# Optimization experiments

Measured on AMD Instinct MI355X. Metric: run time of the kernel, lower is better.

Reference implementation:

```python
import jax, jax.numpy as jnp
import numpy as np

B, S, T, D, H, K, F = 8, 512, 512, 1024, 16, 64, 4096
EPS = 1e-6
NEG = -1e9


def _ln(x, g, b):
    mu = jnp.mean(x, axis=-1, keepdims=True)
    var = jnp.mean(jnp.square(x - mu), axis=-1, keepdims=True)
    return (x - mu) * jax.lax.rsqrt(var + EPS) * g + b


def _mha(q_in, kv_in, wq, bq, wk, bk, wv, bv, wo, bo, mask=None):
    # q_in: [B,S,D], kv_in: [B,T,D]
    q = jnp.einsum('bsd,dhk->bshk', q_in, wq) + bq
    k = jnp.einsum('btd,dhk->bthk', kv_in, wk) + bk
    v = jnp.einsum('btd,dhk->bthk', kv_in, wv) + bv
    scores = jnp.einsum('bshk,bthk->bhst', q, k) / jnp.sqrt(jnp.float32(K))
    if mask is not None:
        scores = jnp.where(mask, scores, NEG)
    attn = jax.nn.softmax(scores, axis=-1)  # [B,H,S,T]
    ctx = jnp.einsum('bhst,bthk->bshk', attn, v)
    out = jnp.einsum('bshk,hkd->bsd', ctx, wo) + bo
    return out, attn


def setup_inputs() -> dict:
    key = jax.random.key(0)
    ks = jax.random.split(key, 24)
    r = lambda i, shape: 0.02 * jax.random.normal(ks[i], shape, dtype=jnp.float32)
    inp = {
        'x': jax.random.normal(ks[0], (B, S, D), dtype=jnp.float32),
        'enc_output': jax.random.normal(ks[1], (B, T, D), dtype=jnp.float32),
        'look_ahead_mask': jnp.tril(jnp.ones((S, S), dtype=bool))[None, None],
        # mha1 (self-attention)
        'wq1': r(2, (D, H, K)), 'bq1': jnp.zeros((H, K), jnp.float32),
        'wk1': r(3, (D, H, K)), 'bk1': jnp.zeros((H, K), jnp.float32),
        'wv1': r(4, (D, H, K)), 'bv1': jnp.zeros((H, K), jnp.float32),
        'wo1': r(5, (H, K, D)), 'bo1': jnp.zeros((D,), jnp.float32),
        # mha2 (cross-attention)
        'wq2': r(6, (D, H, K)), 'bq2': jnp.zeros((H, K), jnp.float32),
        'wk2': r(7, (D, H, K)), 'bk2': jnp.zeros((H, K), jnp.float32),
        'wv2': r(8, (D, H, K)), 'bv2': jnp.zeros((H, K), jnp.float32),
        'wo2': r(9, (H, K, D)), 'bo2': jnp.zeros((D,), jnp.float32),
        # layernorms
        'g1': jnp.ones((D,), jnp.float32), 'be1': jnp.zeros((D,), jnp.float32),
        'g2': jnp.ones((D,), jnp.float32), 'be2': jnp.zeros((D,), jnp.float32),
        'g3': jnp.ones((D,), jnp.float32), 'be3': jnp.zeros((D,), jnp.float32),
        # ffn
        'w_fc1': r(10, (D, F)), 'b_fc1': jnp.zeros((F,), jnp.float32),
        'w_fc2': r(11, (F, D)), 'b_fc2': jnp.zeros((D,), jnp.float32),
    }
    return inp


def reference(x, enc_output, look_ahead_mask,
              wq1, bq1, wk1, bk1, wv1, bv1, wo1, bo1,
              wq2, bq2, wk2, bk2, wv2, bv2, wo2, bo2,
              g1, be1, g2, be2, g3, be3,
              w_fc1, b_fc1, w_fc2, b_fc2):
    attn1, attn_w1 = _mha(x, x, wq1, bq1, wk1, bk1, wv1, bv1, wo1, bo1,
                          mask=look_ahead_mask)
    out1 = _ln(attn1 + x, g1, be1)
    attn2, attn_w2 = _mha(out1, enc_output, wq2, bq2, wk2, bk2, wv2, bv2, wo2, bo2)
    out2 = _ln(attn2 + out1, g2, be2)
    h = jax.nn.relu(jnp.einsum('bsd,df->bsf', out2, w_fc1) + b_fc1)
    out_ffn = jnp.einsum('bsf,fd->bsd', h, w_fc2) + b_fc2
    dec_layer_out = _ln(out_ffn + out2, g3, be3)
    return dec_layer_out, attn_w1, attn_w2
```

## Files before the change

kernel.cpp:

```cpp
#include <hip/hip_runtime.h>

typedef __attribute__((ext_vector_type(4))) float f32x4;
typedef __attribute__((ext_vector_type(8))) __bf16 bf16x8;

__device__ __forceinline__ unsigned short f2b(float f){
  union { float f; unsigned int u; } v; v.f = f;
  unsigned int r = v.u + 0x7FFFu + ((v.u >> 16) & 1u);
  return (unsigned short)(r >> 16);
}
__device__ __forceinline__ float b2f(unsigned short u){
  union { unsigned int u; float f; } v; v.u = ((unsigned int)u) << 16;
  return v.f;
}
__device__ __forceinline__ bool in_is_bf16(const void* g1){
  return ((const unsigned short*)g1)[0] == 0x3F80u;
}

#define GLD16(gp, lp) __builtin_amdgcn_global_load_lds( \
    (const __attribute__((address_space(1))) unsigned int*)(gp), \
    (__attribute__((address_space(3))) unsigned int*)(lp), 16, 0, 0)

__global__ __launch_bounds__(256) void k_fill(float* p, long long n, float v){
  long long i = (long long)blockIdx.x*256 + threadIdx.x;
  long long stride = (long long)gridDim.x*256;
  for(; i < n; i += stride) p[i] = v;
}

struct SmallConv { const void* src[16]; int n[16]; int off[16]; };
struct TW4 { const void* s[4]; };

template<bool SMALL>
__global__ __launch_bounds__(256) void k_prepA(SmallConv sc, float* bias,
    const void* act_in, unsigned short* act_out,
    TW4 tw, unsigned short* wdst, const void* g1f)
{
  __shared__ float tile[32][33];
  bool isb = in_is_bf16(g1f);
  int bi = blockIdx.x, tid = threadIdx.x;
  int base = SMALL ? 16 : 0;
  if(SMALL && bi < 16){
    const void* s = sc.src[bi];
    float* d = bias + sc.off[bi];
    int n = sc.n[bi];
    for(int j=tid;j<n;j+=256)
      d[j] = isb ? b2f(((const unsigned short*)s)[j]) : ((const float*)s)[j];
  } else if(bi < base + 2048){
    for(int i=(bi-base)*256+tid; i<4194304; i+=2048*256){
      float v = isb ? b2f(((const unsigned short*)act_in)[i]) : ((const float*)act_in)[i];
      act_out[i] = f2b(v);
    }
  } else {
    int r = bi - (base + 2048);
    int wi = r >> 10, rem = r & 1023;
    int c0 = (rem & 31)*32, r0 = (rem >> 5)*32;
    const void* src = tw.s[wi];
    unsigned short* dst = wdst + (size_t)wi*1048576;
    int tx = tid & 31, ty = tid >> 5;
    for(int rr=ty; rr<32; rr+=8){
      size_t o = (size_t)(r0+rr)*1024 + c0 + tx;
      tile[rr][tx] = isb ? b2f(((const unsigned short*)src)[o]) : ((const float*)src)[o];
    }
    __syncthreads();
    for(int cc=ty; cc<32; cc+=8)
      dst[(size_t)(c0+cc)*1024 + r0 + tx] = f2b(tile[tx][cc]);
  }
}

__global__ __launch_bounds__(256) void k_prep3(
    const void* fc1, unsigned short* fc1t,
    const void* fc2, unsigned short* fc2t, const void* g1f)
{
  __shared__ float tile[32][33];
  bool isb = in_is_bf16(g1f);
  int bi = blockIdx.x, tid = threadIdx.x;
  const void* src; unsigned short* dst; int R, C, bx, by;
  if(bi < 4096){ src = fc1; dst = fc1t; R = 1024; C = 4096; bx = bi & 127; by = bi >> 7; }
  else { int r = bi - 4096; src = fc2; dst = fc2t; R = 4096; C = 1024; bx = r & 31; by = r >> 5; }
  int c0 = bx*32, r0 = by*32;
  int tx = tid & 31, ty = tid >> 5;
  for(int rr=ty; rr<32; rr+=8){
    size_t o = (size_t)(r0+rr)*C + c0 + tx;
    tile[rr][tx] = isb ? b2f(((const unsigned short*)src)[o]) : ((const float*)src)[o];
  }
  __syncthreads();
  for(int cc=ty; cc<32; cc+=8)
    dst[(size_t)(c0+cc)*R + r0 + tx] = f2b(tile[tx][cc]);
}

template<int EPI>
__global__ __launch_bounds__(256) void k_gemm(
    const unsigned short* __restrict__ A, int lda,
    const unsigned short* __restrict__ Bt, int ldb,
    void* __restrict__ Cout, int ldc,
    const float* __restrict__ bias, const unsigned short* __restrict__ resid, int K)
{
  __shared__ unsigned short As[2][128*32];
  __shared__ unsigned short Bs[2][128*32];
  int tid = threadIdx.x;
  int lane = tid & 63, w = tid >> 6;
  int lr = lane & 15, lg = lane >> 4;
  int m0 = blockIdx.y * 128, n0 = blockIdx.x * 128;
  int wr = w >> 1, wc = w & 1;

  f32x4 acc[4][4];
  #pragma unroll
  for(int m=0;m<4;m++)
    #pragma unroll
    for(int n=0;n<4;n++) acc[m][n] = (f32x4){0.f,0.f,0.f,0.f};

  #pragma unroll
  for(int j=0;j<2;j++){
    int idx = j*256 + tid;
    GLD16(A + (size_t)(m0 + (idx>>2))*lda + (idx&3)*8,
          As[0] + (size_t)(j*256 + (tid & 192))*8);
    GLD16(Bt + (size_t)(n0 + (idx>>2))*ldb + (idx&3)*8,
          Bs[0] + (size_t)(j*256 + (tid & 192))*8);
  }
  __syncthreads();

  int cur = 0;
  for(int k0 = 0; k0 < K; k0 += 32){
    if(k0 + 32 < K){
      #pragma unroll
      for(int j=0;j<2;j++){
        int idx = j*256 + tid;
        GLD16(A + (size_t)(m0 + (idx>>2))*lda + k0 + 32 + (idx&3)*8,
              As[cur^1] + (size_t)(j*256 + (tid & 192))*8);
        GLD16(Bt + (size_t)(n0 + (idx>>2))*ldb + k0 + 32 + (idx&3)*8,
              Bs[cur^1] + (size_t)(j*256 + (tid & 192))*8);
      }
    }
    bf16x8 a[4], b[4];
    #pragma unroll
    for(int m=0;m<4;m++) a[m] = *(const bf16x8*)&As[cur][(wr*64 + m*16 + lr)*32 + lg*8];
    #pragma unroll
    for(int n=0;n<4;n++) b[n] = *(const bf16x8*)&Bs[cur][(wc*64 + n*16 + lr)*32 + lg*8];
    #pragma unroll
    for(int m=0;m<4;m++)
      #pragma unroll
      for(int n=0;n<4;n++)
        acc[m][n] = __builtin_amdgcn_mfma_f32_16x16x32_bf16(a[m], b[n], acc[m][n], 0,0,0);
    __syncthreads();
    cur ^= 1;
  }

  #pragma unroll
  for(int m=0;m<4;m++){
    #pragma unroll
    for(int n=0;n<4;n++){
      int col = n0 + wc*64 + n*16 + lr;
      float bb = bias[col];
      #pragma unroll
      for(int r=0;r<4;r++){
        int row = m0 + wr*64 + m*16 + lg*4 + r;
        size_t o = (size_t)row*ldc + col;
        float v = acc[m][n][r] + bb;
        if constexpr (EPI == 0){
          ((unsigned short*)Cout)[o] = f2b(v);
        } else if constexpr (EPI == 1){
          ((unsigned short*)Cout)[o] = f2b(v > 0.f ? v : 0.f);
        } else if constexpr (EPI == 2){
          ((unsigned short*)Cout)[o] = f2b(v + b2f(resid[o]));
        } else {
          ((float*)Cout)[o] = v + b2f(resid[o]);
        }
      }
    }
  }
}

template<int EPI>
__global__ __launch_bounds__(256) void k_gemm64(
    const unsigned short* __restrict__ A, int lda,
    const unsigned short* __restrict__ Bt, int ldb,
    void* __restrict__ Cout, int ldc,
    const float* __restrict__ bias, const unsigned short* __restrict__ resid, int K)
{
  __shared__ unsigned short As[2][128*32];
  __shared__ unsigned short Bs[2][64*32];
  int tid = threadIdx.x, lane = tid & 63, w = tid >> 6;
  int lr = lane & 15, lg = lane >> 4;
  int m0 = blockIdx.y * 128, n0 = blockIdx.x * 64;

  f32x4 acc[2][4];
  #pragma unroll
  for(int m=0;m<2;m++)
    #pragma unroll
    for(int n=0;n<4;n++) acc[m][n] = (f32x4){0.f,0.f,0.f,0.f};

  #pragma unroll
  for(int j=0;j<2;j++){
    int idx = j*256 + tid;
    GLD16(A + (size_t)(m0 + (idx>>2))*lda + (idx&3)*8,
          As[0] + (size_t)(j*256 + (tid & 192))*8);
  }
  GLD16(Bt + (size_t)(n0 + (tid>>2))*ldb + (tid&3)*8,
        Bs[0] + (size_t)(tid & 192)*8);
  __syncthreads();

  int cur = 0;
  for(int k0 = 0; k0 < K; k0 += 32){
    if(k0 + 32 < K){
      #pragma unroll
      for(int j=0;j<2;j++){
        int idx = j*256 + tid;
        GLD16(A + (size_t)(m0 + (idx>>2))*lda + k0 + 32 + (idx&3)*8,
              As[cur^1] + (size_t)(j*256 + (tid & 192))*8);
      }
      GLD16(Bt + (size_t)(n0 + (tid>>2))*ldb + k0 + 32 + (tid&3)*8,
            Bs[cur^1] + (size_t)(tid & 192)*8);
    }
    bf16x8 a[2], bf[4];
    #pragma unroll
    for(int m=0;m<2;m++) a[m] = *(const bf16x8*)&As[cur][(w*32 + m*16 + lr)*32 + lg*8];
    #pragma unroll
    for(int n=0;n<4;n++) bf[n] = *(const bf16x8*)&Bs[cur][(n*16 + lr)*32 + lg*8];
    #pragma unroll
    for(int m=0;m<2;m++)
      #pragma unroll
      for(int n=0;n<4;n++)
        acc[m][n] = __builtin_amdgcn_mfma_f32_16x16x32_bf16(a[m], bf[n], acc[m][n], 0,0,0);
    __syncthreads();
    cur ^= 1;
  }

  #pragma unroll
  for(int m=0;m<2;m++){
    #pragma unroll
    for(int n=0;n<4;n++){
      int col = n0 + n*16 + lr;
      float bb = bias[col];
      #pragma unroll
      for(int r=0;r<4;r++){
        int row = m0 + w*32 + m*16 + lg*4 + r;
        size_t o = (size_t)row*ldc + col;
        float v = acc[m][n][r] + bb;
        if constexpr (EPI == 0){
          ((unsigned short*)Cout)[o] = f2b(v);
        } else if constexpr (EPI == 1){
          ((unsigned short*)Cout)[o] = f2b(v > 0.f ? v : 0.f);
        } else if constexpr (EPI == 2){
          ((unsigned short*)Cout)[o] = f2b(v + b2f(resid[o]));
        } else {
          ((float*)Cout)[o] = v + b2f(resid[o]);
        }
      }
    }
  }
}

template<int TSLOT>
__global__ __launch_bounds__(256) void k_gemmsplit(
    const unsigned short* __restrict__ A, int lda,
    const unsigned short* __restrict__ Bt, int ldb,
    unsigned short* __restrict__ C0, unsigned short* __restrict__ C1,
    unsigned short* __restrict__ C2,
    const float* __restrict__ bias, int K)
{
  __shared__ unsigned short As[2][128*32];
  __shared__ unsigned short Bs[2][128*32];
  int tid = threadIdx.x;
  int lane = tid & 63, w = tid >> 6;
  int lr = lane & 15, lg = lane >> 4;
  int m0 = blockIdx.y * 128, n0 = blockIdx.x * 128;
  int wr = w >> 1, wc = w & 1;
  int slot = n0 >> 10;
  unsigned short* Cs = slot == 0 ? C0 : (slot == 1 ? C1 : C2);
  int nl0 = n0 & 1023;

  f32x4 acc[4][4];
  #pragma unroll
  for(int m=0;m<4;m++)
    #pragma unroll
    for(int n=0;n<4;n++) acc[m][n] = (f32x4){0.f,0.f,0.f,0.f};

  #pragma unroll
  for(int j=0;j<2;j++){
    int idx = j*256 + tid;
    GLD16(A + (size_t)(m0 + (idx>>2))*lda + (idx&3)*8,
          As[0] + (size_t)(j*256 + (tid & 192))*8);
    GLD16(Bt + (size_t)(n0 + (idx>>2))*ldb + (idx&3)*8,
          Bs[0] + (size_t)(j*256 + (tid & 192))*8);
  }
  __syncthreads();

  int cur = 0;
  for(int k0 = 0; k0 < K; k0 += 32){
    if(k0 + 32 < K){
      #pragma unroll
      for(int j=0;j<2;j++){
        int idx = j*256 + tid;
        GLD16(A + (size_t)(m0 + (idx>>2))*lda + k0 + 32 + (idx&3)*8,
              As[cur^1] + (size_t)(j*256 + (tid & 192))*8);
        GLD16(Bt + (size_t)(n0 + (idx>>2))*ldb + k0 + 32 + (idx&3)*8,
              Bs[cur^1] + (size_t)(j*256 + (tid & 192))*8);
      }
    }
    bf16x8 a[4], b[4];
    #pragma unroll
    for(int m=0;m<4;m++) a[m] = *(const bf16x8*)&As[cur][(wr*64 + m*16 + lr)*32 + lg*8];
    #pragma unroll
    for(int n=0;n<4;n++) b[n] = *(const bf16x8*)&Bs[cur][(wc*64 + n*16 + lr)*32 + lg*8];
    #pragma unroll
    for(int m=0;m<4;m++)
      #pragma unroll
      for(int n=0;n<4;n++)
        acc[m][n] = __builtin_amdgcn_mfma_f32_16x16x32_bf16(a[m], b[n], acc[m][n], 0,0,0);
    __syncthreads();
    cur ^= 1;
  }

  if(slot != TSLOT){
    #pragma unroll
    for(int m=0;m<4;m++){
      #pragma unroll
      for(int n=0;n<4;n++){
        int coll = nl0 + wc*64 + n*16 + lr;
        float bb = bias[n0 + wc*64 + n*16 + lr];
        #pragma unroll
        for(int r=0;r<4;r++){
          int row = m0 + wr*64 + m*16 + lg*4 + r;
          Cs[(size_t)row*1024 + coll] = f2b(acc[m][n][r] + bb);
        }
      }
    }
  } else {
    #pragma unroll
    for(int m=0;m<4;m++){
      #pragma unroll
      for(int n=0;n<4;n++){
        int vcol = nl0 + wc*64 + n*16 + lr;
        float bb = bias[n0 + wc*64 + n*16 + lr];
        int rowb = m0 + wr*64 + m*16 + lg*4;
        int z = (rowb >> 9)*16 + (vcol >> 6);
        unsigned short tmp[4];
        #pragma unroll
        for(int r=0;r<4;r++) tmp[r] = f2b(acc[m][n][r] + bb);
        *(ushort4*)&Cs[((size_t)(z*64 + (vcol & 63)))*512 + (rowb & 511)] = *(ushort4*)tmp;
      }
    }
  }
}

template<bool CAUSAL>
__global__ __launch_bounds__(256) void k_attnf(
    const unsigned short* Q,
    const unsigned short* __restrict__ Km,
    const unsigned short* __restrict__ Vt,
    float* __restrict__ P,
    unsigned short* C)
{
  int tid = threadIdx.x, lane = tid & 63, w = tid >> 6;
  int lr = lane & 15, lg = lane >> 4;
  int s0 = blockIdx.x * 32;
  int h = blockIdx.y, b = blockIdx.z;
  int z = b*16 + h;
  const unsigned short* Qb = Q + ((size_t)(b*512 + s0))*1024 + h*64;
  const unsigned short* Kb = Km + ((size_t)(b*512))*1024 + h*64;
  float* Pb = P + ((size_t)(z*512 + s0))*512;

  __shared__ unsigned short P_lds[32*520];
  __shared__ float redm[32][4];
  __shared__ float reds[32][4];

  bf16x8 aq[2][2];
  #pragma unroll
  for(int m=0;m<2;m++)
    #pragma unroll
    for(int kk=0;kk<2;kk++)
      aq[m][kk] = *(const bf16x8*)(Qb + (size_t)(m*16 + lr)*1024 + kk*32 + lg*8);

  f32x4 sc[2][8];
  #pragma unroll
  for(int m=0;m<2;m++)
    #pragma unroll
    for(int cb=0;cb<8;cb++) sc[m][cb] = (f32x4){0.f,0.f,0.f,0.f};

  #pragma unroll
  for(int cb=0; cb<8; cb++){
    int col = w*128 + cb*16 + lr;
    #pragma unroll
    for(int kk=0; kk<2; kk++){
      bf16x8 bq = *(const bf16x8*)(Kb + (size_t)col*1024 + kk*32 + lg*8);
      #pragma unroll
      for(int m=0;m<2;m++)
        sc[m][cb] = __builtin_amdgcn_mfma_f32_16x16x32_bf16(aq[m][kk], bq, sc[m][cb], 0,0,0);
    }
  }

  #pragma unroll
  for(int m=0;m<2;m++)
    #pragma unroll
    for(int cb=0;cb<8;cb++)
      #pragma unroll
      for(int r=0;r<4;r++){
        int row_l = m*16 + lg*4 + r;
        int col = w*128 + cb*16 + lr;
        float v = sc[m][cb][r] * 0.125f;
        if(CAUSAL && col > s0 + row_l) v = -1e9f;
        sc[m][cb][r] = v;
      }

  float gmax[2][4];
  #pragma unroll
  for(int m=0;m<2;m++)
    #pragma unroll
    for(int r=0;r<4;r++){
      float pm = -1e30f;
      #pragma unroll
      for(int cb=0;cb<8;cb++) pm = fmaxf(pm, sc[m][cb][r]);
      #pragma unroll
      for(int off=1; off<16; off<<=1) pm = fmaxf(pm, __shfl_xor(pm, off));
      if(lr == 0) redm[m*16 + lg*4 + r][w] = pm;
    }
  __syncthreads();
  #pragma unroll
  for(int m=0;m<2;m++)
    #pragma unroll
    for(int r=0;r<4;r++){
      int row_l = m*16 + lg*4 + r;
      gmax[m][r] = fmaxf(fmaxf(redm[row_l][0], redm[row_l][1]),
                         fmaxf(redm[row_l][2], redm[row_l][3]));
    }
  #pragma unroll
  for(int m=0;m<2;m++)
    #pragma unroll
    for(int r=0;r<4;r++){
      float ps = 0.f;
      #pragma unroll
      for(int cb=0;cb<8;cb++){
        float e = __expf(sc[m][cb][r] - gmax[m][r]);
        sc[m][cb][r] = e;
        ps += e;
      }
      #pragma unroll
      for(int off=1; off<16; off<<=1) ps += __shfl_xor(ps, off);
      if(lr == 0) reds[m*16 + lg*4 + r][w] = ps;
    }
  __syncthreads();
  #pragma unroll
  for(int m=0;m<2;m++)
    #pragma unroll
    for(int r=0;r<4;r++){
      int row_l = m*16 + lg*4 + r;
      float inv = 1.f / (reds[row_l][0] + reds[row_l][1] + reds[row_l][2] + reds[row_l][3]);
      #pragma unroll
      for(int cb=0;cb<8;cb++){
        int col = w*128 + cb*16 + lr;
        float p = sc[m][cb][r] * inv;
        Pb[(size_t)row_l*512 + col] = p;
        P_lds[row_l*520 + col] = f2b(p);
      }
    }
  __syncthreads();

  const unsigned short* Vb = Vt + ((size_t)z*64 + w*16 + lr)*512;
  f32x4 pacc[2];
  pacc[0] = (f32x4){0.f,0.f,0.f,0.f};
  pacc[1] = (f32x4){0.f,0.f,0.f,0.f};
  for(int kk = 0; kk < 16; kk++){
    bf16x8 bfrag = *(const bf16x8*)(Vb + kk*32 + lg*8);
    #pragma unroll
    for(int m=0;m<2;m++){
      bf16x8 afrag = *(const bf16x8*)&P_lds[(m*16 + lr)*520 + kk*32 + lg*8];
      pacc[m] = __builtin_amdgcn_mfma_f32_16x16x32_bf16(afrag, bfrag, pacc[m], 0,0,0);
    }
  }
  #pragma unroll
  for(int m=0;m<2;m++)
    #pragma unroll
    for(int r=0;r<4;r++)
      C[((size_t)(b*512 + s0 + m*16 + lg*4 + r))*1024 + h*64 + w*16 + lr] = f2b(pacc[m][r]);
}

template<int F32IN, int F32OUT>
__global__ __launch_bounds__(256) void k_ln(const void* __restrict__ in,
    const float* __restrict__ g, const float* __restrict__ be,
    void* __restrict__ out)
{
  int row = blockIdx.x, tid = threadIdx.x;
  float v[4];
  if constexpr (F32IN){
    f32x4 u = *(const f32x4*)((const float*)in + (size_t)row*1024 + tid*4);
    v[0]=u[0]; v[1]=u[1]; v[2]=u[2]; v[3]=u[3];
  } else {
    uint2 u = *(const uint2*)((const unsigned short*)in + (size_t)row*1024 + tid*4);
    v[0] = b2f(u.x & 0xFFFF); v[1] = b2f(u.x >> 16);
    v[2] = b2f(u.y & 0xFFFF); v[3] = b2f(u.y >> 16);
  }
  float s = v[0]+v[1]+v[2]+v[3];
  float s2 = v[0]*v[0]+v[1]*v[1]+v[2]*v[2]+v[3]*v[3];
  #pragma unroll
  for(int off=1; off<64; off<<=1){ s += __shfl_xor(s, off); s2 += __shfl_xor(s2, off); }
  __shared__ float red[2][4];
  int w = tid >> 6;
  if((tid & 63) == 0){ red[0][w] = s; red[1][w] = s2; }
  __syncthreads();
  s  = red[0][0]+red[0][1]+red[0][2]+red[0][3];
  s2 = red[1][0]+red[1][1]+red[1][2]+red[1][3];
  float mu = s * (1.f/1024.f);
  float var = s2 * (1.f/1024.f) - mu*mu;
  float rstd = rsqrtf(var + 1e-6f);
  int c = tid*4;
  float y0 = (v[0]-mu)*rstd*g[c+0] + be[c+0];
  float y1 = (v[1]-mu)*rstd*g[c+1] + be[c+1];
  float y2 = (v[2]-mu)*rstd*g[c+2] + be[c+2];
  float y3 = (v[3]-mu)*rstd*g[c+3] + be[c+3];
  if constexpr (F32OUT){
    f32x4 o = {y0, y1, y2, y3};
    *(f32x4*)((float*)out + (size_t)row*1024 + c) = o;
  } else {
    unsigned int o0 = (unsigned int)f2b(y0) | ((unsigned int)f2b(y1) << 16);
    unsigned int o1 = (unsigned int)f2b(y2) | ((unsigned int)f2b(y3) << 16);
    *(uint2*)((unsigned short*)out + (size_t)row*1024 + c) = make_uint2(o0, o1);
  }
}

extern "C" void kernel_launch(void* const* d_in, const int* in_sizes, int n_in,
                              void* d_out, int out_size, void* d_ws, size_t ws_size,
                              hipStream_t stream)
{
  float* out0 = (float*)d_out;

  static const int exp_sizes[29] = {
    4194304, 4194304, 262144,
    1048576, 1024, 1048576, 1024, 1048576, 1024, 1048576, 1024,
    1048576, 1024, 1048576, 1024, 1048576, 1024, 1048576, 1024,
    1024, 1024, 1024, 1024, 1024, 1024,
    4194304, 4096, 4194304, 1024 };
  bool ok = (n_in == 29);
  if(ok) for(int i=0;i<29;i++) if(in_sizes[i] != exp_sizes[i]) { ok = false; break; }
  if(!ok){
    k_fill<<<2048,256,0,stream>>>(out0, (long long)out_size, 100.0f);
    return;
  }
  size_t nslots = ws_size > 131072 ? (ws_size - 131072) / 8388608 : 0;
  if(nslots < 5){
    k_fill<<<2048,256,0,stream>>>(out0, (long long)out_size, 200.0f);
    return;
  }
  bool bigws = nslots >= 9;

  const void* g1f = d_in[19];
  char* ws = (char*)d_ws;
  float* bias = (float*)(ws);
  unsigned short* SL[9];
  for(int i=0;i<9;i++) SL[i] = (unsigned short*)(ws + 131072 + (size_t)i*8388608);

  float* P1 = out0 + 4194304;
  float* P2 = P1 + 33554432;

  SmallConv scv;
  const int si[16] = {4,6,8,10,12,14,16,18,19,20,21,22,23,24,26,28};
  const int sn[16] = {1024,1024,1024,1024,1024,1024,1024,1024,
                      1024,1024,1024,1024,1024,1024,4096,1024};
  const int so[16] = {0,1024,2048,3072,4096,5120,6144,7168,
                      8192,9216,10240,11264,12288,13312,14336,18432};
  for(int i=0;i<16;i++){ scv.src[i]=d_in[si[i]]; scv.n[i]=sn[i]; scv.off[i]=so[i]; }

  {
    TW4 tw{}; tw.s[0]=d_in[3]; tw.s[1]=d_in[5]; tw.s[2]=d_in[7]; tw.s[3]=d_in[9];
    k_prepA<true><<<6160,256,0,stream>>>(scv, bias, d_in[0], SL[0], tw, SL[1], g1f);
  }
  k_gemmsplit<2><<<dim3(24,32),256,0,stream>>>(SL[0],1024, SL[1],1024,
                                               SL[2], SL[3], SL[4], bias+0, 1024);
  k_attnf<true><<<dim3(16,16,8),256,0,stream>>>(SL[2], SL[3], SL[4], P1, SL[2]);
  k_gemm64<2><<<dim3(16,32),256,0,stream>>>(SL[2],1024, SL[1]+3145728,1024,
                                            SL[3],1024, bias+3072, SL[0], 1024);
  k_ln<0,0><<<4096,256,0,stream>>>(SL[3], bias+8192, bias+9216, SL[4]);

  {
    TW4 tw{}; tw.s[0]=d_in[11]; tw.s[1]=d_in[13]; tw.s[2]=d_in[15]; tw.s[3]=d_in[17];
    k_prepA<false><<<6144,256,0,stream>>>(scv, bias, d_in[1], SL[0], tw, SL[1], g1f);
  }
  k_gemmsplit<1><<<dim3(16,32),256,0,stream>>>(SL[0],1024, SL[1]+1048576,1024,
                                               SL[2], SL[3], nullptr, bias+5120, 1024);
  k_gemm64<0><<<dim3(16,32),256,0,stream>>>(SL[4],1024, SL[1],1024,
                                            SL[0],1024, bias+4096, nullptr, 1024);
  k_attnf<false><<<dim3(16,16,8),256,0,stream>>>(SL[0], SL[2], SL[3], P2, SL[0]);
  k_gemm64<2><<<dim3(16,32),256,0,stream>>>(SL[0],1024, SL[1]+3145728,1024,
                                            SL[2],1024, bias+7168, SL[4], 1024);
  k_ln<0,0><<<4096,256,0,stream>>>(SL[2], bias+10240, bias+11264, SL[3]);

  k_prep3<<<8192,256,0,stream>>>(d_in[25], SL[4], d_in[27], SL[0], g1f);
  if(bigws){
    unsigned short* H = SL[5];
    k_gemm<1><<<dim3(32,32),256,0,stream>>>(SL[3],1024, SL[4],1024, H,4096, bias+14336, nullptr, 1024);
    k_gemm64<3><<<dim3(16,32),256,0,stream>>>(H,4096, SL[0],4096, out0,1024, bias+18432, SL[3], 4096);
    k_ln<1,1><<<4096,256,0,stream>>>(out0, bias+12288, bias+13312, out0);
  } else {
    unsigned short* H = SL[1];
    for(int c=0;c<2;c++){
      unsigned short* arow = SL[3] + (size_t)c*2097152;
      float* orow = out0 + (size_t)c*2097152;
      k_gemm<1><<<dim3(32,16),256,0,stream>>>(arow,1024, SL[4],1024, H,4096, bias+14336, nullptr, 1024);
      k_gemm64<3><<<dim3(16,16),256,0,stream>>>(H,4096, SL[0],4096, orow,1024, bias+18432, arow, 4096);
      k_ln<1,1><<<2048,256,0,stream>>>(orow, bias+12288, bias+13312, orow);
    }
  }
}
```

Measured before the change: 471.6 us.

## Triple-buffer GEMM LDS staging with explicit vmcnt waits and raw barriers

Converts the three GEMM kernels from double-buffered to triple-buffered LDS staging, prefetching two K-tiles ahead through global_load_lds. The old __syncthreads is replaced by a partial s_waitcnt vmcnt plus s_barrier, so one tile's loads can stay in flight across the barrier. The aim is to hide more global load latency behind MFMA work. In exchange, LDS use rises by half, which may lower occupancy, and correctness now depends on the hand-set vmcnt counts matching the number of loads issued per stage.

```diff
diff --git a/kernel.cpp b/kernel.cpp
--- a/kernel.cpp
+++ b/kernel.cpp
@@ -94,13 +94,14 @@
     void* __restrict__ Cout, int ldc,
     const float* __restrict__ bias, const unsigned short* __restrict__ resid, int K)
 {
-  __shared__ unsigned short As[2][128*32];
-  __shared__ unsigned short Bs[2][128*32];
+  __shared__ unsigned short As[3][128*32];
+  __shared__ unsigned short Bs[3][128*32];
   int tid = threadIdx.x;
   int lane = tid & 63, w = tid >> 6;
   int lr = lane & 15, lg = lane >> 4;
   int m0 = blockIdx.y * 128, n0 = blockIdx.x * 128;
   int wr = w >> 1, wc = w & 1;
+  int nt = K >> 5;
 
   f32x4 acc[4][4];
   #pragma unroll
@@ -108,27 +109,26 @@
     #pragma unroll
     for(int n=0;n<4;n++) acc[m][n] = (f32x4){0.f,0.f,0.f,0.f};
 
-  #pragma unroll
-  for(int j=0;j<2;j++){
-    int idx = j*256 + tid;
-    GLD16(A + (size_t)(m0 + (idx>>2))*lda + (idx&3)*8,
-          As[0] + (size_t)(j*256 + (tid & 192))*8);
-    GLD16(Bt + (size_t)(n0 + (idx>>2))*ldb + (idx&3)*8,
-          Bs[0] + (size_t)(j*256 + (tid & 192))*8);
-  }
-  __syncthreads();
+  #define STAGE_G(kt, sb) { int k0_ = (kt)*32; \
+    _Pragma("unroll") \
+    for(int j=0;j<2;j++){ \
+      int idx = j*256 + tid; \
+      GLD16(A + (size_t)(m0 + (idx>>2))*lda + k0_ + (idx&3)*8, \
+            &As[sb][(size_t)(j*256 + (tid & 192))*8]); \
+      GLD16(Bt + (size_t)(n0 + (idx>>2))*ldb + k0_ + (idx&3)*8, \
+            &Bs[sb][(size_t)(j*256 + (tid & 192))*8]); \
+    } }
+
+  STAGE_G(0, 0);
+  STAGE_G(1, 1);
+  asm volatile("s_waitcnt vmcnt(4)" ::: "memory");
+  __builtin_amdgcn_s_barrier();
 
   int cur = 0;
-  for(int k0 = 0; k0 < K; k0 += 32){
-    if(k0 + 32 < K){
-      #pragma unroll
-      for(int j=0;j<2;j++){
-        int idx = j*256 + tid;
-        GLD16(A + (size_t)(m0 + (idx>>2))*lda + k0 + 32 + (idx&3)*8,
-              As[cur^1] + (size_t)(j*256 + (tid & 192))*8);
-        GLD16(Bt + (size_t)(n0 + (idx>>2))*ldb + k0 + 32 + (idx&3)*8,
-              Bs[cur^1] + (size_t)(j*256 + (tid & 192))*8);
-      }
+  for(int t = 0; t < nt; ++t){
+    if(t + 2 < nt){
+      int sb = cur + 2; if(sb >= 3) sb -= 3;
+      STAGE_G(t+2, sb);
     }
     bf16x8 a[4], b[4];
     #pragma unroll
@@ -140,9 +140,14 @@
       #pragma unroll
       for(int n=0;n<4;n++)
         acc[m][n] = __builtin_amdgcn_mfma_f32_16x16x32_bf16(a[m], b[n], acc[m][n], 0,0,0);
-    __syncthreads();
-    cur ^= 1;
-  }
+    if(t + 1 < nt){
+      if(t + 2 < nt) asm volatile("s_waitcnt lgkmcnt(0) vmcnt(4)" ::: "memory");
+      else           asm volatile("s_waitcnt lgkmcnt(0) vmcnt(0)" ::: "memory");
+      __builtin_amdgcn_s_barrier();
+    }
+    cur = cur + 1; if(cur >= 3) cur -= 3;
+  }
+  #undef STAGE_G
 
   #pragma unroll
   for(int m=0;m<4;m++){
@@ -176,11 +181,12 @@
     void* __restrict__ Cout, int ldc,
     const float* __restrict__ bias, const unsigned short* __restrict__ resid, int K)
 {
-  __shared__ unsigned short As[2][128*32];
-  __shared__ unsigned short Bs[2][64*32];
+  __shared__ unsigned short As[3][128*32];
+  __shared__ unsigned short Bs[3][64*32];
   int tid = threadIdx.x, lane = tid & 63, w = tid >> 6;
   int lr = lane & 15, lg = lane >> 4;
   int m0 = blockIdx.y * 128, n0 = blockIdx.x * 64;
+  int nt = K >> 5;
 
   f32x4 acc[2][4];
   #pragma unroll
@@ -188,27 +194,26 @@
     #pragma unroll
     for(int n=0;n<4;n++) acc[m][n] = (f32x4){0.f,0.f,0.f,0.f};
 
-  #pragma unroll
-  for(int j=0;j<2;j++){
-    int idx = j*256 + tid;
-    GLD16(A + (size_t)(m0 + (idx>>2))*lda + (idx&3)*8,
-          As[0] + (size_t)(j*256 + (tid & 192))*8);
-  }
-  GLD16(Bt + (size_t)(n0 + (tid>>2))*ldb + (tid&3)*8,
-        Bs[0] + (size_t)(tid & 192)*8);
-  __syncthreads();
+  #define STAGE_G64(kt, sb) { int k0_ = (kt)*32; \
+    _Pragma("unroll") \
+    for(int j=0;j<2;j++){ \
+      int idx = j*256 + tid; \
+      GLD16(A + (size_t)(m0 + (idx>>2))*lda + k0_ + (idx&3)*8, \
+            &As[sb][(size_t)(j*256 + (tid & 192))*8]); \
+    } \
+    GLD16(Bt + (size_t)(n0 + (tid>>2))*ldb + k0_ + (tid&3)*8, \
+          &Bs[sb][(size_t)(tid & 192)*8]); }
+
+  STAGE_G64(0, 0);
+  STAGE_G64(1, 1);
+  asm volatile("s_waitcnt vmcnt(3)" ::: "memory");
+  __builtin_amdgcn_s_barrier();
 
   int cur = 0;
-  for(int k0 = 0; k0 < K; k0 += 32){
-    if(k0 + 32 < K){
-      #pragma unroll
-      for(int j=0;j<2;j++){
-        int idx = j*256 + tid;
-        GLD16(A + (size_t)(m0 + (idx>>2))*lda + k0 + 32 + (idx&3)*8,
-              As[cur^1] + (size_t)(j*256 + (tid & 192))*8);
-      }
-      GLD16(Bt + (size_t)(n0 + (tid>>2))*ldb + k0 + 32 + (tid&3)*8,
-            Bs[cur^1] + (size_t)(tid & 192)*8);
+  for(int t = 0; t < nt; ++t){
+    if(t + 2 < nt){
+      int sb = cur + 2; if(sb >= 3) sb -= 3;
+      STAGE_G64(t+2, sb);
     }
     bf16x8 a[2], bf[4];
     #pragma unroll
@@ -220,9 +225,14 @@
       #pragma unroll
       for(int n=0;n<4;n++)
         acc[m][n] = __builtin_amdgcn_mfma_f32_16x16x32_bf16(a[m], bf[n], acc[m][n], 0,0,0);
-    __syncthreads();
-    cur ^= 1;
-  }
+    if(t + 1 < nt){
+      if(t + 2 < nt) asm volatile("s_waitcnt lgkmcnt(0) vmcnt(3)" ::: "memory");
+      else           asm volatile("s_waitcnt lgkmcnt(0) vmcnt(0)" ::: "memory");
+      __builtin_amdgcn_s_barrier();
+    }
+    cur = cur + 1; if(cur >= 3) cur -= 3;
+  }
+  #undef STAGE_G64
 
   #pragma unroll
   for(int m=0;m<2;m++){
@@ -257,8 +267,8 @@
     unsigned short* __restrict__ C2,
     const float* __restrict__ bias, int K)
 {
-  __shared__ unsigned short As[2][128*32];
-  __shared__ unsigned short Bs[2][128*32];
+  __shared__ unsigned short As[3][128*32];
+  __shared__ unsigned short Bs[3][128*32];
   int tid = threadIdx.x;
   int lane = tid & 63, w = tid >> 6;
   int lr = lane & 15, lg = lane >> 4;
@@ -267,6 +277,7 @@
   int slot = n0 >> 10;
   unsigned short* Cs = slot == 0 ? C0 : (slot == 1 ? C1 : C2);
   int nl0 = n0 & 1023;
+  int nt = K >> 5;
 
   f32x4 acc[4][4];
   #pragma unroll
@@ -274,27 +285,26 @@
     #pragma unroll
     for(int n=0;n<4;n++) acc[m][n] = (f32x4){0.f,0.f,0.f,0.f};
 
-  #pragma unroll
-  for(int j=0;j<2;j++){
-    int idx = j*256 + tid;
-    GLD16(A + (size_t)(m0 + (idx>>2))*lda + (idx&3)*8,
-          As[0] + (size_t)(j*256 + (tid & 192))*8);
-    GLD16(Bt + (size_t)(n0 + (idx>>2))*ldb + (idx&3)*8,
-          Bs[0] + (size_t)(j*256 + (tid & 192))*8);
-  }
-  __syncthreads();
+  #define STAGE_GS(kt, sb) { int k0_ = (kt)*32; \
+    _Pragma("unroll") \
+    for(int j=0;j<2;j++){ \
+      int idx = j*256 + tid; \
+      GLD16(A + (size_t)(m0 + (idx>>2))*lda + k0_ + (idx&3)*8, \
+            &As[sb][(size_t)(j*256 + (tid & 192))*8]); \
+      GLD16(Bt + (size_t)(n0 + (idx>>2))*ldb + k0_ + (idx&3)*8, \
+            &Bs[sb][(size_t)(j*256 + (tid & 192))*8]); \
+    } }
+
+  STAGE_GS(0, 0);
+  STAGE_GS(1, 1);
+  asm volatile("s_waitcnt vmcnt(4)" ::: "memory");
+  __builtin_amdgcn_s_barrier();
 
   int cur = 0;
-  for(int k0 = 0; k0 < K; k0 += 32){
-    if(k0 + 32 < K){
-      #pragma unroll
-      for(int j=0;j<2;j++){
-        int idx = j*256 + tid;
-        GLD16(A + (size_t)(m0 + (idx>>2))*lda + k0 + 32 + (idx&3)*8,
-              As[cur^1] + (size_t)(j*256 + (tid & 192))*8);
-        GLD16(Bt + (size_t)(n0 + (idx>>2))*ldb + k0 + 32 + (idx&3)*8,
-              Bs[cur^1] + (size_t)(j*256 + (tid & 192))*8);
-      }
+  for(int t = 0; t < nt; ++t){
+    if(t + 2 < nt){
+      int sb = cur + 2; if(sb >= 3) sb -= 3;
+      STAGE_GS(t+2, sb);
     }
     bf16x8 a[4], b[4];
     #pragma unroll
@@ -306,9 +316,14 @@
       #pragma unroll
       for(int n=0;n<4;n++)
         acc[m][n] = __builtin_amdgcn_mfma_f32_16x16x32_bf16(a[m], b[n], acc[m][n], 0,0,0);
-    __syncthreads();
-    cur ^= 1;
-  }
+    if(t + 1 < nt){
+      if(t + 2 < nt) asm volatile("s_waitcnt lgkmcnt(0) vmcnt(4)" ::: "memory");
+      else           asm volatile("s_waitcnt lgkmcnt(0) vmcnt(0)" ::: "memory");
+      __builtin_amdgcn_s_barrier();
+    }
+    cur = cur + 1; if(cur >= 3) cur -= 3;
+  }
+  #undef STAGE_GS
 
   if(slot != TSLOT){
     #pragma unroll
```

New measurement: 478.5 us. About the same (+1.5%).
